# Kernel tuning notes

Measured on AMD Instinct MI355X. Metric: run time of the kernel, lower is better.

## Reference

```python
import jax, jax.numpy as jnp
import numpy as np
import math

NUM_HEADS = 16


def _alibi_slopes(num_heads: int):
    # geometric sequence for power-of-2 head counts (paper's scheme)
    def slopes_pow2(n):
        start = 2.0 ** (-(2.0 ** (-(math.log2(n) - 3))))
        return [start * (start ** i) for i in range(n)]
    if math.log2(num_heads).is_integer():
        return slopes_pow2(num_heads)
    c = 2 ** math.floor(math.log2(num_heads))
    extra = slopes_pow2(2 * c)[0::2][: num_heads - c]
    return slopes_pow2(c) + extra


def setup_inputs() -> dict:
    key = jax.random.key(0)
    kq, kk, kv = jax.random.split(key, 3)
    B, H, S, D = 2, NUM_HEADS, 2048, 64
    q = jax.random.normal(kq, (B, H, S, D), dtype=jnp.float32)
    k = jax.random.normal(kk, (B, H, S, D), dtype=jnp.float32)
    v = jax.random.normal(kv, (B, H, S, D), dtype=jnp.float32)
    return {"q": q, "k": k, "v": v}


def reference(q, k, v):
    B, H, Sq, D = q.shape
    Sk = k.shape[2]
    slopes = jnp.asarray(_alibi_slopes(H), dtype=jnp.float32)  # [H]
    pos = jnp.arange(Sk)
    # abs relative positions (symmetric, non-causal) as in the source
    rel = jnp.abs(pos[None, :] - pos[:, None]).astype(jnp.float32)  # [Sk, Sk]
    alibi = -slopes[:, None, None] * rel[None, :Sq, :]  # [H, Sq, Sk]
    scores = jnp.einsum("bhqd,bhkd->bhqk", q, k) / math.sqrt(D)
    scores = scores + alibi[None]
    probs = jax.nn.softmax(scores, axis=-1)
    return jnp.einsum("bhqk,bhkd->bhqd", probs, v)
```

## Files before the change

kernel.cpp:

```cpp
#include <hip/hip_runtime.h>
#include <hip/hip_bf16.h>
#include <math.h>

typedef __bf16 bf16;
typedef __attribute__((ext_vector_type(8))) bf16 bf16x8;
typedef __attribute__((ext_vector_type(2))) bf16 bf16x2;
typedef __attribute__((ext_vector_type(16))) float f32x16;
typedef __attribute__((ext_vector_type(4))) unsigned int uint4v;

#define SQ 2048
#define DH 64
#define NH 16
#define KVT 32
#define NKVT (SQ / KVT)
#define REC 8192
#define LOG2E 1.44269504088896340736f

__device__ __forceinline__ float fast_exp2(float x) {
#if __has_builtin(__builtin_amdgcn_exp2f)
    return __builtin_amdgcn_exp2f(x);
#else
    return exp2f(x);
#endif
}

__device__ __forceinline__ unsigned pkbf16(float a, float b) {
    union { bf16x2 h; unsigned u; } x;
    x.h = (bf16x2){(bf16)a, (bf16)b};
    return x.u;
}

#if __has_builtin(__builtin_amdgcn_permlane32_swap)
__device__ __forceinline__ void plswap(unsigned &a, unsigned &b) {
    typedef __attribute__((ext_vector_type(2))) unsigned int uint2v;
    uint2v r = __builtin_amdgcn_permlane32_swap(a, b, false, false);
    a = r[0]; b = r[1];
}
#else
__device__ __forceinline__ void plswap(unsigned &a, unsigned &b) {
    asm volatile("v_permlane32_swap_b32 %0, %1" : "+v"(a), "+v"(b));
}
#endif

union FragU { uint4v u; bf16x8 b; };

__global__ __launch_bounds__(256)
void alibi_prep_kernel(const float* __restrict__ K, const float* __restrict__ V,
                       char* __restrict__ W) {
    __shared__ bf16 lt[64][80];
    const int t  = threadIdx.x;
    const int s0 = blockIdx.x * 64;
    const int bh = blockIdx.y;
    if (blockIdx.z == 0) {
#pragma unroll
        for (int i = 0; i < 2; ++i) {
            const int g    = i * 256 + t;
            const int tile = g >> 8;
            const int cc   = g & 255;
            const int ds   = cc >> 6;
            const int lane = cc & 63;
            const float* p = K + ((size_t)bh * SQ + s0 + tile * 32 + (lane & 31)) * DH
                               + ds * 16 + (lane >> 5) * 8;
            float4 a = *(const float4*)p, b = *(const float4*)(p + 4);
            bf16x8 pk = {(bf16)a.x,(bf16)a.y,(bf16)a.z,(bf16)a.w,
                         (bf16)b.x,(bf16)b.y,(bf16)b.z,(bf16)b.w};
            *(bf16x8*)(W + (size_t)(bh * NKVT + (s0 >> 5) + tile) * REC
                         + ds * 1024 + lane * 16) = pk;
        }
    } else {
#pragma unroll
        for (int i = 0; i < 2; ++i) {
            int idx = i * 256 + t;
            int row = idx >> 3, c8 = idx & 7;
            const float* p = V + ((size_t)bh * SQ + s0 + row) * DH + c8 * 8;
            float4 a = *(const float4*)p, b = *(const float4*)(p + 4);
            bf16 e[8] = {(bf16)a.x,(bf16)a.y,(bf16)a.z,(bf16)a.w,
                         (bf16)b.x,(bf16)b.y,(bf16)b.z,(bf16)b.w};
#pragma unroll
            for (int jj = 0; jj < 8; ++jj) lt[c8 * 8 + jj][row] = e[jj];
        }
        __syncthreads();
#pragma unroll
        for (int i = 0; i < 2; ++i) {
            const int g    = i * 256 + t;
            const int tile = g >> 8;
            const int cc   = g & 255;
            const int grp  = cc >> 6;
            const int lane = cc & 63;
            const int d    = (grp >> 1) * 32 + (lane & 31);
            const int sl   = tile * 32 + (grp & 1) * 16 + (lane >> 5) * 8;
            bf16x8 v = *(const bf16x8*)&lt[d][sl];
            *(bf16x8*)(W + (size_t)(bh * NKVT + (s0 >> 5) + tile) * REC
                         + 4096 + grp * 1024 + lane * 16) = v;
        }
    }
}

__global__ __launch_bounds__(256, 4)
void alibi_attn_kernel(const float* __restrict__ Q, const char* __restrict__ W,
                       float* __restrict__ Out) {
    __shared__ float ex[2][64][33];
    const int tid  = threadIdx.x;
    const int lane = tid & 63;
    const int par  = tid >> 6;
    const int r32  = lane & 31;
    const int hi   = lane >> 5;

    const int B  = blockIdx.x;
    const int x  = B & 7;
    const int j  = B >> 3;
    const int sl = j >> 6;
    const int qc = j & 63;
    const int h  = (sl < 2) ? (15 - x) : x;
    const int bh = (sl & 1) * NH + h;
    const int q0 = qc * 32;

    const float slope2  = exp2f(-0.5f * (float)(h + 1)) * LOG2E;
    const float SLOPE2N = -slope2;
    const float QSCALE  = 0.125f * LOG2E;

    const int D = (int)(24.0f / slope2);
    const int a0 = q0 - D;
    const int tmin = (a0 <= 0) ? 0 : (a0 >> 5);
    const int tmax = min(NKVT - 1, (q0 + 31 + D) >> 5);

    const float* Qp = Q + (size_t)bh * SQ * DH;
    float*       Op = Out + (size_t)bh * SQ * DH;
    const char*  rec = W + (size_t)bh * NKVT * REC;

    const int qrow = q0 + r32;
    bf16x8 qfrag[4];
#pragma unroll
    for (int ds = 0; ds < 4; ++ds) {
        const float* sq = Qp + (size_t)qrow * DH + ds * 16 + hi * 8;
        float4 a = *(const float4*)sq, bb = *(const float4*)(sq + 4);
        qfrag[ds] = (bf16x8){(bf16)(a.x*QSCALE),(bf16)(a.y*QSCALE),
                             (bf16)(a.z*QSCALE),(bf16)(a.w*QSCALE),
                             (bf16)(bb.x*QSCALE),(bf16)(bb.y*QSCALE),
                             (bf16)(bb.z*QSCALE),(bf16)(bb.w*QSCALE)};
    }

    f32x16 oacc[2];
#pragma unroll
    for (int d = 0; d < 2; ++d)
#pragma unroll
        for (int rr = 0; rr < 16; ++rr) oacc[d][rr] = 0.f;
    float ps0 = 0.f, ps1 = 0.f, ps2 = 0.f, ps3 = 0.f;
    const float qh = (float)(qrow - 4 * hi);

    for (int t = tmin + par; t <= tmax; t += 4) {
        const char* rb = rec + (size_t)t * REC;

        bf16x8 kf[4], vf[4];
#pragma unroll
        for (int ds = 0; ds < 4; ++ds)
            kf[ds] = *(const bf16x8*)(rb + ds * 1024 + lane * 16);
#pragma unroll
        for (int g = 0; g < 4; ++g)
            vf[g] = *(const bf16x8*)(rb + 4096 + g * 1024 + lane * 16);

        f32x16 sacc;
#pragma unroll
        for (int rr = 0; rr < 16; ++rr) sacc[rr] = 0.f;
        __builtin_amdgcn_s_setprio(1);
#pragma unroll
        for (int ds = 0; ds < 4; ++ds)
            sacc = __builtin_amdgcn_mfma_f32_32x32x16_bf16(kf[ds], qfrag[ds], sacc, 0, 0, 0);
        __builtin_amdgcn_s_setprio(0);

        const float gq = qh - (float)(t * KVT);
        float p[16];
#pragma unroll
        for (int reg = 0; reg < 16; ++reg) {
            const int krel = (reg & 3) + 8 * (reg >> 2);
            float d = gq - (float)krel;
            float s2 = fmaf(SLOPE2N, fabsf(d), sacc[reg]);
            float e = fast_exp2(s2);
            p[reg] = e;
            if ((reg & 3) == 0) ps0 += e;
            else if ((reg & 3) == 1) ps1 += e;
            else if ((reg & 3) == 2) ps2 += e;
            else ps3 += e;
        }

        __builtin_amdgcn_s_setprio(1);
#pragma unroll
        for (int ks = 0; ks < 2; ++ks) {
            unsigned u0 = pkbf16(p[8 * ks + 0], p[8 * ks + 1]);
            unsigned u1 = pkbf16(p[8 * ks + 2], p[8 * ks + 3]);
            unsigned v0 = pkbf16(p[8 * ks + 4], p[8 * ks + 5]);
            unsigned v1 = pkbf16(p[8 * ks + 6], p[8 * ks + 7]);
            plswap(u0, v0);
            plswap(u1, v1);
            FragU pf; pf.u = (uint4v){u0, u1, v0, v1};
#pragma unroll
            for (int dblk = 0; dblk < 2; ++dblk)
                oacc[dblk] = __builtin_amdgcn_mfma_f32_32x32x16_bf16(vf[dblk * 2 + ks], pf.b, oacc[dblk], 0, 0, 0);
        }
        __builtin_amdgcn_s_setprio(0);
    }

    float psum = (ps0 + ps1) + (ps2 + ps3);
    psum += __shfl_xor(psum, 32);

    if (par & 1) {
        float* s = &ex[par >> 1][lane][0];
#pragma unroll
        for (int dblk = 0; dblk < 2; ++dblk)
#pragma unroll
            for (int g2 = 0; g2 < 4; ++g2)
                *(float4*)(s + dblk * 16 + g2 * 4) =
                    (float4){oacc[dblk][4*g2+0], oacc[dblk][4*g2+1],
                             oacc[dblk][4*g2+2], oacc[dblk][4*g2+3]};
        s[32] = psum;
    }
    __syncthreads();
    if (!(par & 1)) {
        const float* s = &ex[par >> 1][lane][0];
#pragma unroll
        for (int dblk = 0; dblk < 2; ++dblk)
#pragma unroll
            for (int g2 = 0; g2 < 4; ++g2) {
                float4 o = *(const float4*)(s + dblk * 16 + g2 * 4);
                oacc[dblk][4*g2+0] += o.x; oacc[dblk][4*g2+1] += o.y;
                oacc[dblk][4*g2+2] += o.z; oacc[dblk][4*g2+3] += o.w;
            }
        psum += s[32];
    }
    __syncthreads();
    if (par == 2) {
        float* s = &ex[0][lane][0];
#pragma unroll
        for (int dblk = 0; dblk < 2; ++dblk)
#pragma unroll
            for (int g2 = 0; g2 < 4; ++g2)
                *(float4*)(s + dblk * 16 + g2 * 4) =
                    (float4){oacc[dblk][4*g2+0], oacc[dblk][4*g2+1],
                             oacc[dblk][4*g2+2], oacc[dblk][4*g2+3]};
        s[32] = psum;
    }
    __syncthreads();
    if (par == 0) {
        const float* s = &ex[0][lane][0];
#pragma unroll
        for (int dblk = 0; dblk < 2; ++dblk)
#pragma unroll
            for (int g2 = 0; g2 < 4; ++g2) {
                float4 o = *(const float4*)(s + dblk * 16 + g2 * 4);
                oacc[dblk][4*g2+0] += o.x; oacc[dblk][4*g2+1] += o.y;
                oacc[dblk][4*g2+2] += o.z; oacc[dblk][4*g2+3] += o.w;
            }
        psum += s[32];

        const float inv = 1.f / psum;
#pragma unroll
        for (int dblk = 0; dblk < 2; ++dblk)
#pragma unroll
            for (int g2 = 0; g2 < 4; ++g2) {
                float4 o = {oacc[dblk][4*g2+0] * inv, oacc[dblk][4*g2+1] * inv,
                            oacc[dblk][4*g2+2] * inv, oacc[dblk][4*g2+3] * inv};
                *(float4*)(Op + (size_t)qrow * DH + dblk * 32 + g2 * 8 + hi * 4) = o;
            }
    }
}

extern "C" void kernel_launch(void* const* d_in, const int* in_sizes, int n_in,
                              void* d_out, int out_size, void* d_ws, size_t ws_size,
                              hipStream_t stream) {
    const float* q = (const float*)d_in[0];
    const float* k = (const float*)d_in[1];
    const float* v = (const float*)d_in[2];
    float* out = (float*)d_out;
    char* W = (char*)d_ws;
    alibi_prep_kernel<<<dim3(SQ / 64, 2 * NH, 2), dim3(256), 0, stream>>>(k, v, W);
    const int nblk = 2 * NH * (SQ / 32);
    alibi_attn_kernel<<<dim3(nblk), dim3(256), 0, stream>>>(q, W, out);
}
```

Before: 48.83 us.

## Process 64 query rows per block with double-buffered K/V tile loads

Each block now handles two 32-row query subtiles that share every loaded K/V tile, which halves the global K/V traffic per query. The per-wave loop prefetches the next tile into a second register set, with explicit vmcnt waits, so loads overlap compute. The block-to-head mapping is reworked to balance the uneven ALiBi window sizes across the grid, and the launch bound drops to 2 blocks per CU to make room for the extra registers. The costs are half as many blocks, lower occupancy and a larger LDS reduction buffer.

```diff
diff --git a/kernel.cpp b/kernel.cpp
--- a/kernel.cpp
+++ b/kernel.cpp
@@ -88,32 +88,35 @@
             const int grp  = cc >> 6;
             const int lane = cc & 63;
             const int d    = (grp >> 1) * 32 + (lane & 31);
-            const int sl   = tile * 32 + (grp & 1) * 16 + (lane >> 5) * 8;
-            bf16x8 v = *(const bf16x8*)&lt[d][sl];
+            const int sv   = tile * 32 + (grp & 1) * 16 + (lane >> 5) * 8;
+            bf16x8 v = *(const bf16x8*)&lt[d][sv];
             *(bf16x8*)(W + (size_t)(bh * NKVT + (s0 >> 5) + tile) * REC
                          + 4096 + grp * 1024 + lane * 16) = v;
         }
     }
 }
 
-__global__ __launch_bounds__(256, 4)
+__global__ __launch_bounds__(256, 2)
 void alibi_attn_kernel(const float* __restrict__ Q, const char* __restrict__ W,
                        float* __restrict__ Out) {
-    __shared__ float ex[2][64][33];
+    __shared__ float ex[2][64][72];
     const int tid  = threadIdx.x;
     const int lane = tid & 63;
     const int par  = tid >> 6;
     const int r32  = lane & 31;
     const int hi   = lane >> 5;
 
-    const int B  = blockIdx.x;
-    const int x  = B & 7;
-    const int j  = B >> 3;
-    const int sl = j >> 6;
-    const int qc = j & 63;
-    const int h  = (sl < 2) ? (15 - x) : x;
-    const int bh = (sl & 1) * NH + h;
-    const int q0 = qc * 32;
+    const int B   = blockIdx.x;
+    const int x   = B & 7;
+    const int j   = B >> 3;
+    const int sl  = j >> 5;
+    const int qcr = j & 31;
+    const int qc  = (qcr + sl * 8) & 31;
+    const int hs  = x >> 1;
+    const int h   = (sl == 0) ? (15 - hs) : (sl == 1) ? (11 - hs)
+                  : (sl == 2) ? (2 * hs + 1) : (2 * hs);
+    const int bh  = (x & 1) * NH + h;
+    const int q0  = qc * 64;
 
     const float slope2  = exp2f(-0.5f * (float)(h + 1)) * LOG2E;
     const float SLOPE2N = -slope2;
@@ -122,97 +125,143 @@
     const int D = (int)(24.0f / slope2);
     const int a0 = q0 - D;
     const int tmin = (a0 <= 0) ? 0 : (a0 >> 5);
-    const int tmax = min(NKVT - 1, (q0 + 31 + D) >> 5);
+    const int tmax = min(NKVT - 1, (q0 + 63 + D) >> 5);
 
     const float* Qp = Q + (size_t)bh * SQ * DH;
     float*       Op = Out + (size_t)bh * SQ * DH;
     const char*  rec = W + (size_t)bh * NKVT * REC;
 
-    const int qrow = q0 + r32;
-    bf16x8 qfrag[4];
+    const int qrowA = q0 + r32;
+    bf16x8 qfragA[4], qfragB[4];
 #pragma unroll
     for (int ds = 0; ds < 4; ++ds) {
-        const float* sq = Qp + (size_t)qrow * DH + ds * 16 + hi * 8;
-        float4 a = *(const float4*)sq, bb = *(const float4*)(sq + 4);
-        qfrag[ds] = (bf16x8){(bf16)(a.x*QSCALE),(bf16)(a.y*QSCALE),
-                             (bf16)(a.z*QSCALE),(bf16)(a.w*QSCALE),
-                             (bf16)(bb.x*QSCALE),(bf16)(bb.y*QSCALE),
-                             (bf16)(bb.z*QSCALE),(bf16)(bb.w*QSCALE)};
-    }
-
-    f32x16 oacc[2];
-#pragma unroll
-    for (int d = 0; d < 2; ++d)
-#pragma unroll
-        for (int rr = 0; rr < 16; ++rr) oacc[d][rr] = 0.f;
-    float ps0 = 0.f, ps1 = 0.f, ps2 = 0.f, ps3 = 0.f;
-    const float qh = (float)(qrow - 4 * hi);
-
-    for (int t = tmin + par; t <= tmax; t += 4) {
-        const char* rb = rec + (size_t)t * REC;
-
-        bf16x8 kf[4], vf[4];
-#pragma unroll
-        for (int ds = 0; ds < 4; ++ds)
-            kf[ds] = *(const bf16x8*)(rb + ds * 1024 + lane * 16);
-#pragma unroll
-        for (int g = 0; g < 4; ++g)
-            vf[g] = *(const bf16x8*)(rb + 4096 + g * 1024 + lane * 16);
-
-        f32x16 sacc;
-#pragma unroll
-        for (int rr = 0; rr < 16; ++rr) sacc[rr] = 0.f;
-        __builtin_amdgcn_s_setprio(1);
-#pragma unroll
-        for (int ds = 0; ds < 4; ++ds)
-            sacc = __builtin_amdgcn_mfma_f32_32x32x16_bf16(kf[ds], qfrag[ds], sacc, 0, 0, 0);
-        __builtin_amdgcn_s_setprio(0);
-
-        const float gq = qh - (float)(t * KVT);
-        float p[16];
-#pragma unroll
-        for (int reg = 0; reg < 16; ++reg) {
-            const int krel = (reg & 3) + 8 * (reg >> 2);
-            float d = gq - (float)krel;
-            float s2 = fmaf(SLOPE2N, fabsf(d), sacc[reg]);
-            float e = fast_exp2(s2);
-            p[reg] = e;
-            if ((reg & 3) == 0) ps0 += e;
-            else if ((reg & 3) == 1) ps1 += e;
-            else if ((reg & 3) == 2) ps2 += e;
-            else ps3 += e;
-        }
-
-        __builtin_amdgcn_s_setprio(1);
-#pragma unroll
-        for (int ks = 0; ks < 2; ++ks) {
-            unsigned u0 = pkbf16(p[8 * ks + 0], p[8 * ks + 1]);
-            unsigned u1 = pkbf16(p[8 * ks + 2], p[8 * ks + 3]);
-            unsigned v0 = pkbf16(p[8 * ks + 4], p[8 * ks + 5]);
-            unsigned v1 = pkbf16(p[8 * ks + 6], p[8 * ks + 7]);
-            plswap(u0, v0);
-            plswap(u1, v1);
-            FragU pf; pf.u = (uint4v){u0, u1, v0, v1};
-#pragma unroll
-            for (int dblk = 0; dblk < 2; ++dblk)
-                oacc[dblk] = __builtin_amdgcn_mfma_f32_32x32x16_bf16(vf[dblk * 2 + ks], pf.b, oacc[dblk], 0, 0, 0);
-        }
-        __builtin_amdgcn_s_setprio(0);
-    }
-
-    float psum = (ps0 + ps1) + (ps2 + ps3);
-    psum += __shfl_xor(psum, 32);
+        const float* sa = Qp + (size_t)qrowA * DH + ds * 16 + hi * 8;
+        float4 a = *(const float4*)sa, b = *(const float4*)(sa + 4);
+        qfragA[ds] = (bf16x8){(bf16)(a.x*QSCALE),(bf16)(a.y*QSCALE),
+                              (bf16)(a.z*QSCALE),(bf16)(a.w*QSCALE),
+                              (bf16)(b.x*QSCALE),(bf16)(b.y*QSCALE),
+                              (bf16)(b.z*QSCALE),(bf16)(b.w*QSCALE)};
+        const float* sb = sa + 32 * DH;
+        float4 c = *(const float4*)sb, d = *(const float4*)(sb + 4);
+        qfragB[ds] = (bf16x8){(bf16)(c.x*QSCALE),(bf16)(c.y*QSCALE),
+                              (bf16)(c.z*QSCALE),(bf16)(c.w*QSCALE),
+                              (bf16)(d.x*QSCALE),(bf16)(d.y*QSCALE),
+                              (bf16)(d.z*QSCALE),(bf16)(d.w*QSCALE)};
+    }
+
+    f32x16 oaccA[2], oaccB[2];
+#pragma unroll
+    for (int d2 = 0; d2 < 2; ++d2)
+#pragma unroll
+        for (int rr = 0; rr < 16; ++rr) { oaccA[d2][rr] = 0.f; oaccB[d2][rr] = 0.f; }
+    float psA[4] = {0.f,0.f,0.f,0.f}, psB[4] = {0.f,0.f,0.f,0.f};
+    const float qhA = (float)(qrowA - 4 * hi);
+
+    auto LOADF = [&](bf16x8* kf, bf16x8* vf, int tt) {
+        const char* rb = rec + (size_t)tt * REC + lane * 16;
+#pragma unroll
+        for (int ds = 0; ds < 4; ++ds) kf[ds] = *(const bf16x8*)(rb + ds * 1024);
+#pragma unroll
+        for (int g = 0; g < 4; ++g)    vf[g] = *(const bf16x8*)(rb + 4096 + g * 1024);
+    };
+
+    auto COMPUTE = [&](const bf16x8* kf, const bf16x8* vf, int tt) {
+        const float gq0 = qhA - (float)(tt * KVT);
+#pragma unroll
+        for (int qs = 0; qs < 2; ++qs) {
+            const bf16x8* qf = qs ? qfragB : qfragA;
+            f32x16*       oa = qs ? oaccB  : oaccA;
+            float*        ps = qs ? psB    : psA;
+            const float   gq = qs ? gq0 + 32.f : gq0;
+
+            f32x16 sacc;
+#pragma unroll
+            for (int rr = 0; rr < 16; ++rr) sacc[rr] = 0.f;
+            __builtin_amdgcn_s_setprio(1);
+#pragma unroll
+            for (int ds = 0; ds < 4; ++ds)
+                sacc = __builtin_amdgcn_mfma_f32_32x32x16_bf16(kf[ds], qf[ds], sacc, 0, 0, 0);
+            __builtin_amdgcn_s_setprio(0);
+
+            float p[16];
+#pragma unroll
+            for (int reg = 0; reg < 16; ++reg) {
+                const int krel = (reg & 3) + 8 * (reg >> 2);
+                float d = gq - (float)krel;
+                float s2 = fmaf(SLOPE2N, fabsf(d), sacc[reg]);
+                float e = fast_exp2(s2);
+                p[reg] = e;
+                ps[reg & 3] += e;
+            }
+
+            __builtin_amdgcn_s_setprio(1);
+#pragma unroll
+            for (int ks = 0; ks < 2; ++ks) {
+                unsigned u0 = pkbf16(p[8 * ks + 0], p[8 * ks + 1]);
+                unsigned u1 = pkbf16(p[8 * ks + 2], p[8 * ks + 3]);
+                unsigned v0 = pkbf16(p[8 * ks + 4], p[8 * ks + 5]);
+                unsigned v1 = pkbf16(p[8 * ks + 6], p[8 * ks + 7]);
+                plswap(u0, v0);
+                plswap(u1, v1);
+                FragU pf; pf.u = (uint4v){u0, u1, v0, v1};
+#pragma unroll
+                for (int dblk = 0; dblk < 2; ++dblk)
+                    oa[dblk] = __builtin_amdgcn_mfma_f32_32x32x16_bf16(vf[dblk * 2 + ks], pf.b, oa[dblk], 0, 0, 0);
+            }
+            __builtin_amdgcn_s_setprio(0);
+        }
+    };
+
+    {
+        bf16x8 kA[4], vA[4], kB[4], vB[4];
+        int t = tmin + par;
+        if (t <= tmax) {
+            const int n = ((tmax - t) >> 2) + 1;
+            LOADF(kA, vA, t);
+            int i = 0;
+            while (i + 2 <= n) {
+                LOADF(kB, vB, t + 4);
+                asm volatile("s_waitcnt vmcnt(8)" ::: "memory");
+                __builtin_amdgcn_sched_barrier(0);
+                COMPUTE(kA, vA, t);
+                if (i + 2 < n) {
+                    LOADF(kA, vA, t + 8);
+                    asm volatile("s_waitcnt vmcnt(8)" ::: "memory");
+                } else {
+                    asm volatile("s_waitcnt vmcnt(0)" ::: "memory");
+                }
+                __builtin_amdgcn_sched_barrier(0);
+                COMPUTE(kB, vB, t + 4);
+                t += 8; i += 2;
+            }
+            if (i < n) {
+                asm volatile("s_waitcnt vmcnt(0)" ::: "memory");
+                __builtin_amdgcn_sched_barrier(0);
+                COMPUTE(kA, vA, t);
+            }
+        }
+    }
+
+    float psumA = (psA[0] + psA[1]) + (psA[2] + psA[3]);
+    psumA += __shfl_xor(psumA, 32);
+    float psumB = (psB[0] + psB[1]) + (psB[2] + psB[3]);
+    psumB += __shfl_xor(psumB, 32);
 
     if (par & 1) {
         float* s = &ex[par >> 1][lane][0];
 #pragma unroll
         for (int dblk = 0; dblk < 2; ++dblk)
 #pragma unroll
-            for (int g2 = 0; g2 < 4; ++g2)
+            for (int g2 = 0; g2 < 4; ++g2) {
                 *(float4*)(s + dblk * 16 + g2 * 4) =
-                    (float4){oacc[dblk][4*g2+0], oacc[dblk][4*g2+1],
-                             oacc[dblk][4*g2+2], oacc[dblk][4*g2+3]};
-        s[32] = psum;
+                    (float4){oaccA[dblk][4*g2+0], oaccA[dblk][4*g2+1],
+                             oaccA[dblk][4*g2+2], oaccA[dblk][4*g2+3]};
+                *(float4*)(s + 36 + dblk * 16 + g2 * 4) =
+                    (float4){oaccB[dblk][4*g2+0], oaccB[dblk][4*g2+1],
+                             oaccB[dblk][4*g2+2], oaccB[dblk][4*g2+3]};
+            }
+        s[32] = psumA;
+        s[68] = psumB;
     }
     __syncthreads();
     if (!(par & 1)) {
@@ -221,11 +270,15 @@
         for (int dblk = 0; dblk < 2; ++dblk)
 #pragma unroll
             for (int g2 = 0; g2 < 4; ++g2) {
-                float4 o = *(const float4*)(s + dblk * 16 + g2 * 4);
-                oacc[dblk][4*g2+0] += o.x; oacc[dblk][4*g2+1] += o.y;
-                oacc[dblk][4*g2+2] += o.z; oacc[dblk][4*g2+3] += o.w;
-            }
-        psum += s[32];
+                float4 oa = *(const float4*)(s + dblk * 16 + g2 * 4);
+                float4 ob = *(const float4*)(s + 36 + dblk * 16 + g2 * 4);
+                oaccA[dblk][4*g2+0] += oa.x; oaccA[dblk][4*g2+1] += oa.y;
+                oaccA[dblk][4*g2+2] += oa.z; oaccA[dblk][4*g2+3] += oa.w;
+                oaccB[dblk][4*g2+0] += ob.x; oaccB[dblk][4*g2+1] += ob.y;
+                oaccB[dblk][4*g2+2] += ob.z; oaccB[dblk][4*g2+3] += ob.w;
+            }
+        psumA += s[32];
+        psumB += s[68];
     }
     __syncthreads();
     if (par == 2) {
@@ -233,11 +286,16 @@
 #pragma unroll
         for (int dblk = 0; dblk < 2; ++dblk)
 #pragma unroll
-            for (int g2 = 0; g2 < 4; ++g2)
+            for (int g2 = 0; g2 < 4; ++g2) {
                 *(float4*)(s + dblk * 16 + g2 * 4) =
-                    (float4){oacc[dblk][4*g2+0], oacc[dblk][4*g2+1],
-                             oacc[dblk][4*g2+2], oacc[dblk][4*g2+3]};
-        s[32] = psum;
+                    (float4){oaccA[dblk][4*g2+0], oaccA[dblk][4*g2+1],
+                             oaccA[dblk][4*g2+2], oaccA[dblk][4*g2+3]};
+                *(float4*)(s + 36 + dblk * 16 + g2 * 4) =
+                    (float4){oaccB[dblk][4*g2+0], oaccB[dblk][4*g2+1],
+                             oaccB[dblk][4*g2+2], oaccB[dblk][4*g2+3]};
+            }
+        s[32] = psumA;
+        s[68] = psumB;
     }
     __syncthreads();
     if (par == 0) {
@@ -246,20 +304,28 @@
         for (int dblk = 0; dblk < 2; ++dblk)
 #pragma unroll
             for (int g2 = 0; g2 < 4; ++g2) {
-                float4 o = *(const float4*)(s + dblk * 16 + g2 * 4);
-                oacc[dblk][4*g2+0] += o.x; oacc[dblk][4*g2+1] += o.y;
-                oacc[dblk][4*g2+2] += o.z; oacc[dblk][4*g2+3] += o.w;
-            }
-        psum += s[32];
-
-        const float inv = 1.f / psum;
-#pragma unroll
-        for (int dblk = 0; dblk < 2; ++dblk)
-#pragma unroll
-            for (int g2 = 0; g2 < 4; ++g2) {
-                float4 o = {oacc[dblk][4*g2+0] * inv, oacc[dblk][4*g2+1] * inv,
-                            oacc[dblk][4*g2+2] * inv, oacc[dblk][4*g2+3] * inv};
-                *(float4*)(Op + (size_t)qrow * DH + dblk * 32 + g2 * 8 + hi * 4) = o;
+                float4 oa = *(const float4*)(s + dblk * 16 + g2 * 4);
+                float4 ob = *(const float4*)(s + 36 + dblk * 16 + g2 * 4);
+                oaccA[dblk][4*g2+0] += oa.x; oaccA[dblk][4*g2+1] += oa.y;
+                oaccA[dblk][4*g2+2] += oa.z; oaccA[dblk][4*g2+3] += oa.w;
+                oaccB[dblk][4*g2+0] += ob.x; oaccB[dblk][4*g2+1] += ob.y;
+                oaccB[dblk][4*g2+2] += ob.z; oaccB[dblk][4*g2+3] += ob.w;
+            }
+        psumA += s[32];
+        psumB += s[68];
+
+        const float invA = 1.f / psumA;
+        const float invB = 1.f / psumB;
+#pragma unroll
+        for (int dblk = 0; dblk < 2; ++dblk)
+#pragma unroll
+            for (int g2 = 0; g2 < 4; ++g2) {
+                float4 oa = {oaccA[dblk][4*g2+0] * invA, oaccA[dblk][4*g2+1] * invA,
+                             oaccA[dblk][4*g2+2] * invA, oaccA[dblk][4*g2+3] * invA};
+                *(float4*)(Op + (size_t)qrowA * DH + dblk * 32 + g2 * 8 + hi * 4) = oa;
+                float4 ob = {oaccB[dblk][4*g2+0] * invB, oaccB[dblk][4*g2+1] * invB,
+                             oaccB[dblk][4*g2+2] * invB, oaccB[dblk][4*g2+3] * invB};
+                *(float4*)(Op + (size_t)(qrowA + 32) * DH + dblk * 32 + g2 * 8 + hi * 4) = ob;
             }
     }
 }
@@ -273,6 +339,6 @@
     float* out = (float*)d_out;
     char* W = (char*)d_ws;
     alibi_prep_kernel<<<dim3(SQ / 64, 2 * NH, 2), dim3(256), 0, stream>>>(k, v, W);
-    const int nblk = 2 * NH * (SQ / 32);
+    const int nblk = 2 * NH * (SQ / 64);
     alibi_attn_kernel<<<dim3(nblk), dim3(256), 0, stream>>>(q, W, out);
 }
```

Measured after the change: 46.65 us. 1.05x faster.
